# Optimization experiments

Measured on AMD Instinct MI355X. Metric: run time of the kernel, lower is better.

## Reference

```python
import jax, jax.numpy as jnp
from jax import lax
import numpy as np

B, T, I, H, O = 64, 1024, 256, 512, 128


def setup_inputs() -> dict:
    key = jax.random.key(0)
    ks = jax.random.split(key, 12)
    s_i = 1.0 / np.sqrt(H)
    return {
        "x": jax.random.normal(ks[0], (B, T, I), dtype=jnp.float32),
        "h0": jnp.zeros((2, B, H), dtype=jnp.float32),
        # layer 0 RNNCell(I -> H)
        "W_ih0": jax.random.uniform(ks[1], (H, I), jnp.float32, -s_i, s_i),
        "b_ih0": jax.random.uniform(ks[2], (H,), jnp.float32, -s_i, s_i),
        "W_hh0": jax.random.uniform(ks[3], (H, H), jnp.float32, -s_i, s_i),
        "b_hh0": jax.random.uniform(ks[4], (H,), jnp.float32, -s_i, s_i),
        # layer 1 RNNCell(H -> H)
        "W_ih1": jax.random.uniform(ks[5], (H, H), jnp.float32, -s_i, s_i),
        "b_ih1": jax.random.uniform(ks[6], (H,), jnp.float32, -s_i, s_i),
        "W_hh1": jax.random.uniform(ks[7], (H, H), jnp.float32, -s_i, s_i),
        "b_hh1": jax.random.uniform(ks[8], (H,), jnp.float32, -s_i, s_i),
        # final Linear(H -> O) applied to last timestep hidden
        "W_out": jax.random.uniform(ks[9], (O, H), jnp.float32, -s_i, s_i),
        "b_out": jax.random.uniform(ks[10], (O,), jnp.float32, -s_i, s_i),
    }


def reference(x, h0, W_ih0, b_ih0, W_hh0, b_hh0, W_ih1, b_ih1, W_hh1, b_hh1, W_out, b_out):
    # x: [B, T, I]; h0: [2, B, H]. Stacked tanh RNN cells over time, then
    # Linear head on the last timestep's top-layer hidden (outs[-1]).
    def step(carry, x_t):
        h_0, h_1 = carry  # each [B, H]
        h_0 = jnp.tanh(x_t @ W_ih0.T + b_ih0 + h_0 @ W_hh0.T + b_hh0)
        h_1 = jnp.tanh(h_0 @ W_ih1.T + b_ih1 + h_1 @ W_hh1.T + b_hh1)
        return (h_0, h_1), None

    x_tbi = jnp.swapaxes(x, 0, 1)  # [T, B, I] for scan over time
    (h_0, h_1), _ = lax.scan(step, (h0[0], h0[1]), x_tbi)
    out = h_1 @ W_out.T + b_out  # [B, O]
    return out
```

## Files before the change

### kernel.cpp

```cpp
#include <hip/hip_runtime.h>
#include <hip/hip_bf16.h>

#define TT 1024
#define BB 64
#define II 256
#define HH 512
#define OO 128

typedef __attribute__((ext_vector_type(4))) float f32x4;
typedef __attribute__((ext_vector_type(4))) int   i32x4;
typedef __attribute__((ext_vector_type(2))) unsigned long long u64x2;
typedef __attribute__((ext_vector_type(8))) __bf16 bf16x8;
typedef __attribute__((ext_vector_type(8))) short s16x8;
typedef unsigned long long u64;
typedef unsigned short u16;
typedef unsigned int u32;

#define BIAS_OFF 132096
#define SMEM_BYTES 132608

static __device__ __forceinline__ u16 f2b(float f) { return __builtin_bit_cast(u16, (__bf16)f); }
static __device__ __forceinline__ float b2f(u16 u) { return (float)__builtin_bit_cast(__bf16, u); }

static __device__ __forceinline__ u64 pack4f(float a, float b, float c, float d) {
    return (u64)f2b(a) | ((u64)f2b(b) << 16) | ((u64)f2b(c) << 32) | ((u64)f2b(d) << 48);
}
static __device__ __forceinline__ bf16x8 cvt8(f32x4 a0, f32x4 a1) {
    bf16x8 v;
    v[0]=(__bf16)a0[0]; v[1]=(__bf16)a0[1]; v[2]=(__bf16)a0[2]; v[3]=(__bf16)a0[3];
    v[4]=(__bf16)a1[0]; v[5]=(__bf16)a1[1]; v[6]=(__bf16)a1[2]; v[7]=(__bf16)a1[3];
    return v;
}
static __device__ __forceinline__ bf16x8 mk8(u64 lo, u64 hi) {
    u64x2 v; v[0] = lo; v[1] = hi;
    return __builtin_bit_cast(bf16x8, v);
}
static __device__ __forceinline__ int ald32(const int* p) {
    return __hip_atomic_load(p, __ATOMIC_RELAXED, __HIP_MEMORY_SCOPE_AGENT);
}
static __device__ __forceinline__ u64 ald(const u64* p) {
    return __hip_atomic_load(p, __ATOMIC_RELAXED, __HIP_MEMORY_SCOPE_AGENT);
}
static __device__ __forceinline__ void ast(u64* p, u64 v) {
    __hip_atomic_store(p, v, __ATOMIC_RELAXED, __HIP_MEMORY_SCOPE_AGENT);
}

__global__ __launch_bounds__(512, 2) void xproj_kernel(
    const float* __restrict__ x, const float* __restrict__ Wih0,
    const float* __restrict__ bih0, const float* __restrict__ bhh0,
    u64* __restrict__ XBu)
{
    const int tid = threadIdx.x;
    const int l = tid & 63, w = tid >> 6;
    const int lm = l & 15, lg = l >> 4;
    const int t = blockIdx.x * 4 + (w >> 1);
    const int nh = w & 1;

    bf16x8 xf[4][8];
    #pragma unroll
    for (int bt = 0; bt < 4; ++bt) {
        const float* xb = x + (size_t)(bt * 16 + lm) * (TT * II) + (size_t)t * II + lg * 8;
        #pragma unroll
        for (int kt = 0; kt < 8; ++kt) {
            f32x4 a0 = *(const f32x4*)(xb + kt * 32);
            f32x4 a1 = *(const f32x4*)(xb + kt * 32 + 4);
            xf[bt][kt] = cvt8(a0, a1);
        }
    }
    for (int nt = 0; nt < 16; ++nt) {
        const int n_row = nh * 256 + nt * 16 + lm;
        bf16x8 wf[8];
        #pragma unroll
        for (int kt = 0; kt < 8; ++kt) {
            const float* wsrc = Wih0 + (size_t)n_row * II + kt * 32 + lg * 8;
            f32x4 a0 = *(const f32x4*)(wsrc);
            f32x4 a1 = *(const f32x4*)(wsrc + 4);
            wf[kt] = cvt8(a0, a1);
        }
        f32x4 acc[4] = {{0,0,0,0},{0,0,0,0},{0,0,0,0},{0,0,0,0}};
        #pragma unroll
        for (int kt = 0; kt < 8; ++kt)
            #pragma unroll
            for (int bt = 0; bt < 4; ++bt)
                acc[bt] = __builtin_amdgcn_mfma_f32_16x16x32_bf16(wf[kt], xf[bt][kt], acc[bt], 0, 0, 0);
        const int n0 = nh * 256 + nt * 16 + lg * 4;
        f32x4 bias = *(const f32x4*)(bih0 + n0);
        f32x4 bias2 = *(const f32x4*)(bhh0 + n0);
        #pragma unroll
        for (int bt = 0; bt < 4; ++bt) {
            const int b = bt * 16 + lm;
            XBu[((size_t)t * 64 + b) * 128 + (n0 >> 2)] =
                pack4f(acc[bt][0] + bias[0] + bias2[0], acc[bt][1] + bias[1] + bias2[1],
                       acc[bt][2] + bias[2] + bias2[2], acc[bt][3] + bias[3] + bias2[3]);
        }
    }
}

template <int L>
static __device__ void run_layer(const u16* __restrict__ XB,
                                 const float* __restrict__ hinit,
                                 const float* __restrict__ Wi,
                                 const float* __restrict__ Wh,
                                 const float* __restrict__ bi, const float* __restrict__ bh,
                                 int* cnt0, int* cnt1,
                                 u64* h0s, u64* h1s,
                                 int nb, char* smem)
{
    constexpr int WKG = (L == 0) ? 2 : 4;
    constexpr int MTW = (L == 0) ? 1 : 2;

    const int tid = threadIdx.x;
    const int l = tid & 63, w = tid >> 6;
    const int lm = l & 15, lg = l >> 4;
    const int wm = (L == 0) ? (w & 3) : (w & 1);
    const int wk = (L == 0) ? (w >> 2) : (w >> 1);
    u64* wbase = (L == 0) ? h0s : h1s;
    int* mycnt = (L == 0) ? cnt0 : cnt1;

    {
        const int m = tid >> 3, c8 = tid & 7;
        const float* s = hinit + (size_t)m * HH + nb + c8 * 8;
        u64* d = &wbase[3 * 8192 + m * 128 + (nb >> 2) + c8 * 2];
        ast(&d[0], pack4f(s[0], s[1], s[2], s[3]));
        ast(&d[1], pack4f(s[4], s[5], s[6], s[7]));
    }
    if (L == 1 && tid < 64)
        ((float*)(smem + BIAS_OFF))[tid] = bi[nb + tid] + bh[nb + tid];
    asm volatile("s_waitcnt vmcnt(0)" ::: "memory");
    __syncthreads();
    if (tid == 0)
        __hip_atomic_fetch_add(mycnt, 1, __ATOMIC_RELAXED, __HIP_MEMORY_SCOPE_AGENT);

    bf16x8 B[4][8];
    #pragma unroll
    for (int nt = 0; nt < 4; ++nt) {
        const int n = nb + nt * 16 + lm;
        #pragma unroll
        for (int ktl = 0; ktl < 8; ++ktl) {
            const int ktg = wk * 8 + ktl;
            const float* src;
            if (L == 0) src = Wi + (size_t)n * HH + ktg * 32 + lg * 8;
            else        src = (ktg < 16) ? (Wi + (size_t)n * HH + ktg * 32 + lg * 8)
                                         : (Wh + (size_t)n * HH + (ktg - 16) * 32 + lg * 8);
            f32x4 a0 = *(const f32x4*)(src);
            f32x4 a1 = *(const f32x4*)(src + 4);
            B[nt][ktl] = cvt8(a0, a1);
        }
    }

    float* part = (float*)smem;

    for (int t = 0; t < TT; ++t) {
        f32x4 acc[MTW][4];
        #pragma unroll
        for (int i = 0; i < MTW; ++i)
            #pragma unroll
            for (int nt = 0; nt < 4; ++nt) acc[i][nt] = f32x4{0, 0, 0, 0};

        if (L == 0) {
            const int tgt = 8 * (t + 1);
            while (ald32(cnt0) < tgt) {}
            if (t >= 4) { const int tg1 = 8 * (t - 2); while (ald32(cnt1) < tg1) {} }
            asm volatile("" ::: "memory");
            const u64* sp = h0s + ((t + 3) & 3) * 8192
                          + (wm * 16 + lm) * 128 + wk * 64 + lg * 2;
            u64 pa[8][2];
            #pragma unroll
            for (int ktl = 0; ktl < 8; ++ktl) {
                pa[ktl][0] = ald(sp + ktl * 8);
                pa[ktl][1] = ald(sp + ktl * 8 + 1);
            }
            #pragma unroll
            for (int ktl = 0; ktl < 8; ++ktl) {
                bf16x8 a = mk8(pa[ktl][0], pa[ktl][1]);
                #pragma unroll
                for (int nt = 0; nt < 4; ++nt)
                    acc[0][nt] = __builtin_amdgcn_mfma_f32_16x16x32_bf16(a, B[nt][ktl], acc[0][nt], 0, 0, 0);
            }
        } else {
            if (wk >= 2) {
                const int tgt = 8 * (t + 1);
                while (ald32(cnt1) < tgt) {}
                asm volatile("" ::: "memory");
                const u64* sp = h1s + ((t + 3) & 3) * 8192 + (wk - 2) * 64 + lg * 2;
                #pragma unroll
                for (int i = 0; i < MTW; ++i) {
                    const u64* spm = sp + ((wm * 2 + i) * 16 + lm) * 128;
                    u64 pa[8][2];
                    #pragma unroll
                    for (int ktl = 0; ktl < 8; ++ktl) {
                        pa[ktl][0] = ald(spm + ktl * 8);
                        pa[ktl][1] = ald(spm + ktl * 8 + 1);
                    }
                    #pragma unroll
                    for (int ktl = 0; ktl < 8; ++ktl) {
                        bf16x8 a = mk8(pa[ktl][0], pa[ktl][1]);
                        #pragma unroll
                        for (int nt = 0; nt < 4; ++nt)
                            acc[i][nt] = __builtin_amdgcn_mfma_f32_16x16x32_bf16(a, B[nt][ktl], acc[i][nt], 0, 0, 0);
                    }
                }
            } else {
                const int tgt = 8 * (t + 2);
                while (ald32(cnt0) < tgt) {}
                asm volatile("" ::: "memory");
                const u64* sp = h0s + (t & 3) * 8192 + wk * 64 + lg * 2;
                #pragma unroll
                for (int i = 0; i < MTW; ++i) {
                    const u64* spm = sp + ((wm * 2 + i) * 16 + lm) * 128;
                    u64 pa[8][2];
                    #pragma unroll
                    for (int ktl = 0; ktl < 8; ++ktl) {
                        pa[ktl][0] = ald(spm + ktl * 8);
                        pa[ktl][1] = ald(spm + ktl * 8 + 1);
                    }
                    #pragma unroll
                    for (int ktl = 0; ktl < 8; ++ktl) {
                        bf16x8 a = mk8(pa[ktl][0], pa[ktl][1]);
                        #pragma unroll
                        for (int nt = 0; nt < 4; ++nt)
                            acc[i][nt] = __builtin_amdgcn_mfma_f32_16x16x32_bf16(a, B[nt][ktl], acc[i][nt], 0, 0, 0);
                    }
                }
            }
        }

        #pragma unroll
        for (int i = 0; i < MTW; ++i)
            #pragma unroll
            for (int nt = 0; nt < 4; ++nt)
                #pragma unroll
                for (int r = 0; r < 4; ++r) {
                    const int m = (wm * MTW + i) * 16 + lg * 4 + r;
                    part[(wk * 64 + m) * 64 + nt * 16 + lm] = acc[i][nt][r];
                }
        __syncthreads();

        {
            const int m = tid >> 3, c0 = (tid & 7) * 8;
            f32x4 sa = {0, 0, 0, 0}, sb = {0, 0, 0, 0};
            #pragma unroll
            for (int k = 0; k < WKG; ++k) {
                const float* pr = part + (k * 64 + m) * 64 + c0;
                sa += *(const f32x4*)pr;
                sb += *(const f32x4*)(pr + 4);
            }
            float e[8];
            if (L == 0) {
                const s16x8 xv = *(const s16x8*)(XB + ((size_t)t * 64 + m) * 512 + nb + c0);
                #pragma unroll
                for (int r = 0; r < 4; ++r) {
                    e[r] = sa[r] + b2f((u16)xv[r]);
                    e[4 + r] = sb[r] + b2f((u16)xv[4 + r]);
                }
            } else {
                const float* bl = (const float*)(smem + BIAS_OFF) + c0;
                #pragma unroll
                for (int r = 0; r < 4; ++r) {
                    e[r] = sa[r] + bl[r];
                    e[4 + r] = sb[r] + bl[4 + r];
                }
            }
            u64* d = &wbase[(t & 3) * 8192 + m * 128 + (nb >> 2) + (tid & 7) * 2];
            ast(&d[0], pack4f(tanhf(e[0]), tanhf(e[1]), tanhf(e[2]), tanhf(e[3])));
            ast(&d[1], pack4f(tanhf(e[4]), tanhf(e[5]), tanhf(e[6]), tanhf(e[7])));
        }
        asm volatile("s_waitcnt vmcnt(0)" ::: "memory");
        __syncthreads();
        if (tid == 0)
            __hip_atomic_fetch_add(mycnt, 1, __ATOMIC_RELAXED, __HIP_MEMORY_SCOPE_AGENT);
    }
}

static __device__ void head_phase(const float* __restrict__ Wout,
                                  const float* __restrict__ bout,
                                  const u64* __restrict__ h1slot,
                                  float* __restrict__ out,
                                  int obase, int* cnt1, char* smem)
{
    const int tid = threadIdx.x;
    if (tid == 0) { while (ald32(cnt1) < 8 * (TT + 1)) {} }
    __syncthreads();
    asm volatile("" ::: "memory");
    float* hf = (float*)smem;
    for (int q = tid; q < 8192; q += 512) {
        u64 v = ald(&h1slot[q]);
        const int m = q >> 7, c4 = (q & 127) * 4;
        float* d = hf + m * 516 + c4;
        d[0] = b2f((u16)v);         d[1] = b2f((u16)(v >> 16));
        d[2] = b2f((u16)(v >> 32)); d[3] = b2f((u16)(v >> 48));
    }
    __syncthreads();
    const int b = tid >> 3, oo = tid & 7;
    const float* hrow = hf + b * 516;
    #pragma unroll
    for (int h = 0; h < 2; ++h) {
        const int o = obase + oo + h * 8;
        const float* wr = Wout + (size_t)o * HH;
        float acc = 0.f;
        #pragma unroll 4
        for (int k4 = 0; k4 < 128; ++k4) {
            f32x4 wv = *(const f32x4*)(wr + k4 * 4);
            f32x4 hv = *(const f32x4*)(hrow + k4 * 4);
            acc += wv[0]*hv[0] + wv[1]*hv[1] + wv[2]*hv[2] + wv[3]*hv[3];
        }
        out[b * OO + o] = acc + bout[o];
    }
}

__global__ __launch_bounds__(512, 2) void rnn_persist(
    const u16* __restrict__ XB,
    const float* __restrict__ h0init,
    const float* __restrict__ Whh0,
    const float* __restrict__ Wih1, const float* __restrict__ bih1,
    const float* __restrict__ Whh1, const float* __restrict__ bhh1,
    const float* __restrict__ Wout, const float* __restrict__ bout,
    float* __restrict__ out, int* __restrict__ cnt, u64* __restrict__ hbuf)
{
    __shared__ __align__(16) char smem[SMEM_BYTES];
    const int bx = blockIdx.x;
    int* cnt0 = cnt;
    int* cnt1 = cnt + 32;
    u64* h0s = hbuf;
    u64* h1s = hbuf + 4 * 8192;
    if (bx < 8) {
        run_layer<0>(XB, h0init, Whh0, nullptr, nullptr, nullptr,
                     cnt0, cnt1, h0s, h1s, bx * 64, smem);
    } else {
        run_layer<1>(nullptr, h0init + BB * HH, Wih1, Whh1, bih1, bhh1,
                     cnt0, cnt1, h0s, h1s, (bx - 8) * 64, smem);
        head_phase(Wout, bout, h1s + 3 * 8192, out, (bx - 8) * 16, cnt1, smem);
    }
}

extern "C" void kernel_launch(void* const* d_in, const int* in_sizes, int n_in,
                              void* d_out, int out_size, void* d_ws, size_t ws_size,
                              hipStream_t stream) {
    const float* x     = (const float*)d_in[0];
    const float* h0i   = (const float*)d_in[1];
    const float* Wih0  = (const float*)d_in[2];
    const float* bih0  = (const float*)d_in[3];
    const float* Whh0  = (const float*)d_in[4];
    const float* bhh0  = (const float*)d_in[5];
    const float* Wih1  = (const float*)d_in[6];
    const float* bih1  = (const float*)d_in[7];
    const float* Whh1  = (const float*)d_in[8];
    const float* bhh1  = (const float*)d_in[9];
    const float* Wout  = (const float*)d_in[10];
    const float* bout  = (const float*)d_in[11];
    float* out = (float*)d_out;

    int* cnt  = (int*)d_ws;
    u64* hbuf = (u64*)((char*)d_ws + 256);
    u16* XB   = (u16*)((char*)d_ws + (1 << 20));

    hipMemsetAsync(d_ws, 0, 256, stream);
    xproj_kernel<<<256, 512, 0, stream>>>(x, Wih0, bih0, bhh0, (u64*)XB);

    void* args[] = { &XB, &h0i, &Whh0, &Wih1, &bih1, &Whh1, &bhh1,
                     &Wout, &bout, &out, &cnt, &hbuf };
    hipLaunchCooperativeKernel((const void*)rnn_persist, dim3(16), dim3(512),
                               args, 0, stream);
}
```

Baseline: 9.572 ms.

## Pack layer counters into one u64, spin on lane 0 with sleep, widen stores

```diff
diff --git a/kernel.cpp b/kernel.cpp
--- a/kernel.cpp
+++ b/kernel.cpp
@@ -35,14 +35,22 @@
     u64x2 v; v[0] = lo; v[1] = hi;
     return __builtin_bit_cast(bf16x8, v);
 }
-static __device__ __forceinline__ int ald32(const int* p) {
-    return __hip_atomic_load(p, __ATOMIC_RELAXED, __HIP_MEMORY_SCOPE_AGENT);
-}
 static __device__ __forceinline__ u64 ald(const u64* p) {
     return __hip_atomic_load(p, __ATOMIC_RELAXED, __HIP_MEMORY_SCOPE_AGENT);
 }
-static __device__ __forceinline__ void ast(u64* p, u64 v) {
-    __hip_atomic_store(p, v, __ATOMIC_RELAXED, __HIP_MEMORY_SCOPE_AGENT);
+static __device__ __forceinline__ void ast16(u64* p, u64 lo, u64 hi) {
+    u64x2 v; v[0] = lo; v[1] = hi;
+    asm volatile("global_store_dwordx4 %0, %1, off sc0 sc1" :: "v"(p), "v"(v) : "memory");
+}
+static __device__ __forceinline__ void spin_pair(const u64* cp, int tgt0, int tgt1, int lane) {
+    if (lane == 0) {
+        for (;;) {
+            u64 v = ald(cp);
+            if ((int)(u32)v >= tgt0 && (int)(u32)(v >> 32) >= tgt1) break;
+            __builtin_amdgcn_s_sleep(1);
+        }
+    }
+    asm volatile("" ::: "memory");
 }
 
 __global__ __launch_bounds__(512, 2) void xproj_kernel(
@@ -102,7 +110,7 @@
                                  const float* __restrict__ Wi,
                                  const float* __restrict__ Wh,
                                  const float* __restrict__ bi, const float* __restrict__ bh,
-                                 int* cnt0, int* cnt1,
+                                 int* cnt0, const u64* cpair,
                                  u64* h0s, u64* h1s,
                                  int nb, char* smem)
 {
@@ -115,14 +123,13 @@
     const int wm = (L == 0) ? (w & 3) : (w & 1);
     const int wk = (L == 0) ? (w >> 2) : (w >> 1);
     u64* wbase = (L == 0) ? h0s : h1s;
-    int* mycnt = (L == 0) ? cnt0 : cnt1;
+    int* mycnt = cnt0 + L;
 
     {
         const int m = tid >> 3, c8 = tid & 7;
         const float* s = hinit + (size_t)m * HH + nb + c8 * 8;
-        u64* d = &wbase[3 * 8192 + m * 128 + (nb >> 2) + c8 * 2];
-        ast(&d[0], pack4f(s[0], s[1], s[2], s[3]));
-        ast(&d[1], pack4f(s[4], s[5], s[6], s[7]));
+        ast16(&wbase[3 * 8192 + m * 128 + (nb >> 2) + c8 * 2],
+              pack4f(s[0], s[1], s[2], s[3]), pack4f(s[4], s[5], s[6], s[7]));
     }
     if (L == 1 && tid < 64)
         ((float*)(smem + BIAS_OFF))[tid] = bi[nb + tid] + bh[nb + tid];
@@ -157,11 +164,12 @@
             #pragma unroll
             for (int nt = 0; nt < 4; ++nt) acc[i][nt] = f32x4{0, 0, 0, 0};
 
+        s16x8 xv;
+        if (L == 0)
+            xv = *(const s16x8*)(XB + ((size_t)t * 64 + (tid >> 3)) * 512 + nb + (tid & 7) * 8);
+
         if (L == 0) {
-            const int tgt = 8 * (t + 1);
-            while (ald32(cnt0) < tgt) {}
-            if (t >= 4) { const int tg1 = 8 * (t - 2); while (ald32(cnt1) < tg1) {} }
-            asm volatile("" ::: "memory");
+            spin_pair(cpair, 8 * (t + 1), (t >= 4) ? 8 * (t - 2) : 0, l);
             const u64* sp = h0s + ((t + 3) & 3) * 8192
                           + (wm * 16 + lm) * 128 + wk * 64 + lg * 2;
             u64 pa[8][2];
@@ -178,49 +186,29 @@
                     acc[0][nt] = __builtin_amdgcn_mfma_f32_16x16x32_bf16(a, B[nt][ktl], acc[0][nt], 0, 0, 0);
             }
         } else {
+            const u64* sp;
             if (wk >= 2) {
-                const int tgt = 8 * (t + 1);
-                while (ald32(cnt1) < tgt) {}
-                asm volatile("" ::: "memory");
-                const u64* sp = h1s + ((t + 3) & 3) * 8192 + (wk - 2) * 64 + lg * 2;
-                #pragma unroll
-                for (int i = 0; i < MTW; ++i) {
-                    const u64* spm = sp + ((wm * 2 + i) * 16 + lm) * 128;
-                    u64 pa[8][2];
+                spin_pair(cpair, 0, 8 * (t + 1), l);
+                sp = h1s + ((t + 3) & 3) * 8192 + (wk - 2) * 64 + lg * 2;
+            } else {
+                spin_pair(cpair, 8 * (t + 2), 0, l);
+                sp = h0s + (t & 3) * 8192 + wk * 64 + lg * 2;
+            }
+            #pragma unroll
+            for (int i = 0; i < MTW; ++i) {
+                const u64* spm = sp + ((wm * 2 + i) * 16 + lm) * 128;
+                u64 pa[8][2];
+                #pragma unroll
+                for (int ktl = 0; ktl < 8; ++ktl) {
+                    pa[ktl][0] = ald(spm + ktl * 8);
+                    pa[ktl][1] = ald(spm + ktl * 8 + 1);
+                }
+                #pragma unroll
+                for (int ktl = 0; ktl < 8; ++ktl) {
+                    bf16x8 a = mk8(pa[ktl][0], pa[ktl][1]);
                     #pragma unroll
-                    for (int ktl = 0; ktl < 8; ++ktl) {
-                        pa[ktl][0] = ald(spm + ktl * 8);
-                        pa[ktl][1] = ald(spm + ktl * 8 + 1);
-                    }
-                    #pragma unroll
-                    for (int ktl = 0; ktl < 8; ++ktl) {
-                        bf16x8 a = mk8(pa[ktl][0], pa[ktl][1]);
-                        #pragma unroll
-                        for (int nt = 0; nt < 4; ++nt)
-                            acc[i][nt] = __builtin_amdgcn_mfma_f32_16x16x32_bf16(a, B[nt][ktl], acc[i][nt], 0, 0, 0);
-                    }
-                }
-            } else {
-                const int tgt = 8 * (t + 2);
-                while (ald32(cnt0) < tgt) {}
-                asm volatile("" ::: "memory");
-                const u64* sp = h0s + (t & 3) * 8192 + wk * 64 + lg * 2;
-                #pragma unroll
-                for (int i = 0; i < MTW; ++i) {
-                    const u64* spm = sp + ((wm * 2 + i) * 16 + lm) * 128;
-                    u64 pa[8][2];
-                    #pragma unroll
-                    for (int ktl = 0; ktl < 8; ++ktl) {
-                        pa[ktl][0] = ald(spm + ktl * 8);
-                        pa[ktl][1] = ald(spm + ktl * 8 + 1);
-                    }
-                    #pragma unroll
-                    for (int ktl = 0; ktl < 8; ++ktl) {
-                        bf16x8 a = mk8(pa[ktl][0], pa[ktl][1]);
-                        #pragma unroll
-                        for (int nt = 0; nt < 4; ++nt)
-                            acc[i][nt] = __builtin_amdgcn_mfma_f32_16x16x32_bf16(a, B[nt][ktl], acc[i][nt], 0, 0, 0);
-                    }
+                    for (int nt = 0; nt < 4; ++nt)
+                        acc[i][nt] = __builtin_amdgcn_mfma_f32_16x16x32_bf16(a, B[nt][ktl], acc[i][nt], 0, 0, 0);
                 }
             }
         }
@@ -247,7 +235,6 @@
             }
             float e[8];
             if (L == 0) {
-                const s16x8 xv = *(const s16x8*)(XB + ((size_t)t * 64 + m) * 512 + nb + c0);
                 #pragma unroll
                 for (int r = 0; r < 4; ++r) {
                     e[r] = sa[r] + b2f((u16)xv[r]);
@@ -261,9 +248,9 @@
                     e[4 + r] = sb[r] + bl[4 + r];
                 }
             }
-            u64* d = &wbase[(t & 3) * 8192 + m * 128 + (nb >> 2) + (tid & 7) * 2];
-            ast(&d[0], pack4f(tanhf(e[0]), tanhf(e[1]), tanhf(e[2]), tanhf(e[3])));
-            ast(&d[1], pack4f(tanhf(e[4]), tanhf(e[5]), tanhf(e[6]), tanhf(e[7])));
+            ast16(&wbase[(t & 3) * 8192 + m * 128 + (nb >> 2) + (tid & 7) * 2],
+                  pack4f(tanhf(e[0]), tanhf(e[1]), tanhf(e[2]), tanhf(e[3])),
+                  pack4f(tanhf(e[4]), tanhf(e[5]), tanhf(e[6]), tanhf(e[7])));
         }
         asm volatile("s_waitcnt vmcnt(0)" ::: "memory");
         __syncthreads();
@@ -276,12 +263,11 @@
                                   const float* __restrict__ bout,
                                   const u64* __restrict__ h1slot,
                                   float* __restrict__ out,
-                                  int obase, int* cnt1, char* smem)
+                                  int obase, const u64* cpair, char* smem)
 {
     const int tid = threadIdx.x;
-    if (tid == 0) { while (ald32(cnt1) < 8 * (TT + 1)) {} }
+    spin_pair(cpair, 0, 8 * (TT + 1), tid);
     __syncthreads();
-    asm volatile("" ::: "memory");
     float* hf = (float*)smem;
     for (int q = tid; q < 8192; q += 512) {
         u64 v = ald(&h1slot[q]);
@@ -319,17 +305,16 @@
 {
     __shared__ __align__(16) char smem[SMEM_BYTES];
     const int bx = blockIdx.x;
-    int* cnt0 = cnt;
-    int* cnt1 = cnt + 32;
+    const u64* cpair = (const u64*)cnt;
     u64* h0s = hbuf;
     u64* h1s = hbuf + 4 * 8192;
     if (bx < 8) {
         run_layer<0>(XB, h0init, Whh0, nullptr, nullptr, nullptr,
-                     cnt0, cnt1, h0s, h1s, bx * 64, smem);
+                     cnt, cpair, h0s, h1s, bx * 64, smem);
     } else {
         run_layer<1>(nullptr, h0init + BB * HH, Wih1, Whh1, bih1, bhh1,
-                     cnt0, cnt1, h0s, h1s, (bx - 8) * 64, smem);
-        head_phase(Wout, bout, h1s + 3 * 8192, out, (bx - 8) * 16, cnt1, smem);
+                     cnt, cpair, h0s, h1s, (bx - 8) * 64, smem);
+        head_phase(Wout, bout, h1s + 3 * 8192, out, (bx - 8) * 16, cpair, smem);
     }
 }
 
```

New measurement: 9.973 ms. +4.2%, slower.
